# Performance work log

Hardware: AMD Instinct MI355X
Metric: run time of the kernel (lower is better)

The kernel has to match this reference:

```python
import jax, jax.numpy as jnp
import numpy as np

CUTOFF = 5.0
COULOMB_CONSTANT = 14.3996454784936  # eV * Angstrom / e^2
SQRT2 = 1.4142135623730951
N_NODES = 500000
N_EDGES = 16000000


def polynomial_cutoff(r, cutoff):
    ratio = r / cutoff
    f = 1.0 - 6.0 * ratio**5 + 15.0 * ratio**4 - 10.0 * ratio**3
    return jnp.where(r <= cutoff, f, 0.0)


def setup_inputs() -> dict:
    key = jax.random.key(0)
    k1, k2, k3, k4, k5 = jax.random.split(key, 5)
    charge = jax.random.normal(k1, (N_NODES,), dtype=jnp.float32)
    # sigma in (0.5, 1.5): positive Gaussian widths
    sigma = jax.random.uniform(k2, (N_NODES,), dtype=jnp.float32) + 0.5
    # bond_dist in (0.1, CUTOFF)
    bond_dist = jax.random.uniform(k3, (N_EDGES,), dtype=jnp.float32) * (CUTOFF - 0.1) + 0.1
    src = jax.random.randint(k4, (N_EDGES,), 0, N_NODES, dtype=jnp.int32)
    dst = jax.random.randint(k5, (N_EDGES,), 0, N_NODES, dtype=jnp.int32)
    return {"charge": charge, "sigma": sigma, "bond_dist": bond_dist, "src": src, "dst": dst}


def reference(charge, sigma, bond_dist, src, dst):
    # Edge-wise message: q_dst * erf(r / (sqrt2 * gamma)) * fcut(r) / r * K
    gamma = jnp.sqrt(sigma[src] ** 2 + sigma[dst] ** 2)  # [E]
    msg = (
        charge[dst]
        * jax.scipy.special.erf(bond_dist / (SQRT2 * gamma))
        * polynomial_cutoff(bond_dist, CUTOFF)
        / bond_dist
    ) * COULOMB_CONSTANT
    # Sum-aggregate messages at destination nodes (DGL fn.sum semantics)
    elec_pot = jax.ops.segment_sum(msg, dst, num_segments=charge.shape[0])
    return elec_pot
```

## Files before the change

### kernel.cpp

```cpp
#include <hip/hip_runtime.h>
#include <hip/hip_fp16.h>
#include <math.h>
#include <stdint.h>

#define CUTOFF_F     5.0f
#define INV_CUTOFF   0.2f
#define KCOUL        14.3996454784936f
#define INV_SQRT2    0.7071067811865475f

typedef int            vint4    __attribute__((ext_vector_type(4)));
typedef float          vfloat4  __attribute__((ext_vector_type(4)));
typedef uint32_t       vuint4   __attribute__((ext_vector_type(4)));
typedef unsigned short vushort8 __attribute__((ext_vector_type(8)));

#define WSHIFT        12
#define WINDOW        4096
#define NB            123
#define WGS_PER_B     8
#define NWG2          (NB * WGS_PER_B)
#define EPT           8
#define EPB           4096
#define OFFS_STRIDE   128
#define SPAN_MAX      512

__device__ __forceinline__ float erf_approx(float x) {
    const float a1 = 0.254829592f, a2 = -0.284496736f, a3 = 1.421413741f,
                a4 = -1.453152027f, a5 = 1.061405429f, p = 0.3275911f;
    float t = __builtin_amdgcn_rcpf(fmaf(p, x, 1.0f));
    float poly = t * fmaf(t, fmaf(t, fmaf(t, fmaf(t, a5, a4), a3), a2), a1);
    return 1.0f - poly * __expf(-x * x);
}

__device__ __forceinline__ float edge_val(float rr, float s2sum) {
    float inv_gamma = rsqrtf(s2sum);
    float x  = rr * INV_CUTOFF;
    float fc = fmaf(x * x * x, fmaf(x, fmaf(-6.0f, x, 15.0f), -10.0f), 1.0f);
    fc = (rr <= CUTOFF_F) ? fc : 0.0f;
    return erf_approx(rr * INV_SQRT2 * inv_gamma) * fc * KCOUL
         * __builtin_amdgcn_rcpf(rr);
}

__global__ __launch_bounds__(256, 6) void p1_bin(
    const float* __restrict__ bond,
    const int*   __restrict__ src,
    const int*   __restrict__ dst,
    unsigned short* __restrict__ offs,
    uint32_t*       __restrict__ sl_out,
    unsigned short* __restrict__ r_out,
    int n_edges)
{
    __shared__ uint32_t hist[NB];
    __shared__ uint32_t scan_s[NB + 1];
    __shared__ alignas(16) uint32_t       buf_sl[EPB];
    __shared__ alignas(16) unsigned short buf_r[EPB];

    const int tid = threadIdx.x;
    const int e0  = blockIdx.x * EPB;

    if (tid < NB) hist[tid] = 0;
    __syncthreads();

    int   dA[EPT], sA[EPT], dB[EPT], sB[EPT];
    float rA[EPT], rB[EPT];
    const bool full = (e0 + EPB <= n_edges);
    if (full) {
        const vint4*   dp = (const vint4*)(dst + e0) + tid;
        const vint4*   sp = (const vint4*)(src + e0) + tid;
        const vfloat4* rp = (const vfloat4*)(bond + e0) + tid;
        vint4 d0 = __builtin_nontemporal_load(dp);
        vint4 d1 = __builtin_nontemporal_load(dp + 256);
        vint4 s0 = __builtin_nontemporal_load(sp);
        vint4 s1 = __builtin_nontemporal_load(sp + 256);
        vfloat4 r0 = __builtin_nontemporal_load(rp);
        vfloat4 r1 = __builtin_nontemporal_load(rp + 256);
        vint4 d2 = __builtin_nontemporal_load(dp + 512);
        vint4 d3 = __builtin_nontemporal_load(dp + 768);
        vint4 s2 = __builtin_nontemporal_load(sp + 512);
        vint4 s3 = __builtin_nontemporal_load(sp + 768);
        vfloat4 r2 = __builtin_nontemporal_load(rp + 512);
        vfloat4 r3 = __builtin_nontemporal_load(rp + 768);
        dA[0]=d0.x; dA[1]=d0.y; dA[2]=d0.z; dA[3]=d0.w;
        dA[4]=d1.x; dA[5]=d1.y; dA[6]=d1.z; dA[7]=d1.w;
        sA[0]=s0.x; sA[1]=s0.y; sA[2]=s0.z; sA[3]=s0.w;
        sA[4]=s1.x; sA[5]=s1.y; sA[6]=s1.z; sA[7]=s1.w;
        rA[0]=r0.x; rA[1]=r0.y; rA[2]=r0.z; rA[3]=r0.w;
        rA[4]=r1.x; rA[5]=r1.y; rA[6]=r1.z; rA[7]=r1.w;
        dB[0]=d2.x; dB[1]=d2.y; dB[2]=d2.z; dB[3]=d2.w;
        dB[4]=d3.x; dB[5]=d3.y; dB[6]=d3.z; dB[7]=d3.w;
        sB[0]=s2.x; sB[1]=s2.y; sB[2]=s2.z; sB[3]=s2.w;
        sB[4]=s3.x; sB[5]=s3.y; sB[6]=s3.z; sB[7]=s3.w;
        rB[0]=r2.x; rB[1]=r2.y; rB[2]=r2.z; rB[3]=r2.w;
        rB[4]=r3.x; rB[5]=r3.y; rB[6]=r3.z; rB[7]=r3.w;
    } else {
        #pragma unroll
        for (int j = 0; j < EPT; ++j) {
            int eA = e0 + (j >> 2) * 1024 + tid * 4 + (j & 3);
            int eB = eA + 2048;
            if (eA < n_edges) { dA[j] = dst[eA]; sA[j] = src[eA]; rA[j] = bond[eA]; }
            else dA[j] = -1;
            if (eB < n_edges) { dB[j] = dst[eB]; sB[j] = src[eB]; rB[j] = bond[eB]; }
            else dB[j] = -1;
        }
    }

    uint32_t slA[EPT], brA[EPT], slB[EPT], brB[EPT];
    unsigned short hrA[EPT], hrB[EPT];
    #pragma unroll
    for (int j = 0; j < EPT; ++j) {
        if (dA[j] >= 0) {
            unsigned b = (unsigned)dA[j] >> WSHIFT;
            uint32_t r = atomicAdd(&hist[b], 1u);
            brA[j] = (b << 16) | r;
            slA[j] = ((uint32_t)sA[j] << WSHIFT) | ((unsigned)dA[j] & (WINDOW - 1));
            hrA[j] = __half_as_ushort(__float2half_rn(rA[j]));
        } else brA[j] = 0xFFFFFFFFu;
    }
    #pragma unroll
    for (int j = 0; j < EPT; ++j) {
        if (dB[j] >= 0) {
            unsigned b = (unsigned)dB[j] >> WSHIFT;
            uint32_t r = atomicAdd(&hist[b], 1u);
            brB[j] = (b << 16) | r;
            slB[j] = ((uint32_t)sB[j] << WSHIFT) | ((unsigned)dB[j] & (WINDOW - 1));
            hrB[j] = __half_as_ushort(__float2half_rn(rB[j]));
        } else brB[j] = 0xFFFFFFFFu;
    }
    __syncthreads();

    if (tid < 64) {
        int i0 = 2 * tid, i1 = 2 * tid + 1;
        uint32_t v0 = (i0 < NB) ? hist[i0] : 0u;
        uint32_t v1 = (i1 < NB) ? hist[i1] : 0u;
        uint32_t s  = v0 + v1;
        uint32_t inc = s;
        #pragma unroll
        for (int d = 1; d < 64; d <<= 1) {
            uint32_t up = __shfl_up(inc, d, 64);
            if (tid >= d) inc += up;
        }
        uint32_t excl = inc - s;
        if (i0 < NB) scan_s[i0] = excl;
        if (i1 < NB) scan_s[i1] = excl + v0;
        if (tid == 63) scan_s[NB] = inc;
    }
    __syncthreads();

    #pragma unroll
    for (int j = 0; j < EPT; ++j)
        if (brA[j] != 0xFFFFFFFFu) {
            uint32_t p = scan_s[brA[j] >> 16] + (brA[j] & 0xFFFFu);
            buf_sl[p] = slA[j]; buf_r[p] = hrA[j];
        }
    #pragma unroll
    for (int j = 0; j < EPT; ++j)
        if (brB[j] != 0xFFFFFFFFu) {
            uint32_t p = scan_s[brB[j] >> 16] + (brB[j] & 0xFFFFu);
            buf_sl[p] = slB[j]; buf_r[p] = hrB[j];
        }
    __syncthreads();

    if (tid <= NB)
        offs[(size_t)blockIdx.x * OFFS_STRIDE + tid] = (unsigned short)scan_s[tid];

    {
        const vuint4* bs = (const vuint4*)buf_sl;
        vuint4* os = (vuint4*)(sl_out + (size_t)blockIdx.x * EPB);
        #pragma unroll
        for (int i = 0; i < EPB / 4 / 256; ++i)
            __builtin_nontemporal_store(bs[tid + i * 256], os + tid + i * 256);
        const vushort8* br = (const vushort8*)buf_r;
        vushort8* orr = (vushort8*)(r_out + (size_t)blockIdx.x * EPB);
        #pragma unroll
        for (int i = 0; i < EPB / 8 / 256; ++i)
            __builtin_nontemporal_store(br[tid + i * 256], orr + tid + i * 256);
    }
}

__global__ __launch_bounds__(256) void p2_acc(
    const uint32_t*       __restrict__ sl_in,
    const unsigned short* __restrict__ r_in,
    const unsigned short* __restrict__ offs,
    const float*          __restrict__ sigma,
    float*                __restrict__ partials,
    int n_nodes, int nblk)
{
    __shared__ float acc[WINDOW];
    __shared__ float sig[WINDOW];
    __shared__ unsigned short offLo[SPAN_MAX];
    __shared__ unsigned short offHi[SPAN_MAX];

    const int g = blockIdx.x;
    const int b = g / WGS_PER_B;
    const int w = g % WGS_PER_B;

    vfloat4* accv = (vfloat4*)acc;
    for (int i = threadIdx.x; i < WINDOW / 4; i += 256)
        accv[i] = (vfloat4){0.f, 0.f, 0.f, 0.f};

    const int nbase  = b << WSHIFT;
    const int nvalid = (n_nodes - nbase < WINDOW) ? (n_nodes - nbase) : WINDOW;
    if (nvalid == WINDOW) {
        vfloat4* sv = (vfloat4*)sig;
        const vfloat4* gp = (const vfloat4*)(sigma + nbase);
        for (int i = threadIdx.x; i < WINDOW / 4; i += 256) sv[i] = gp[i];
    } else {
        for (int i = threadIdx.x; i < WINDOW; i += 256)
            sig[i] = (i < nvalid) ? sigma[nbase + i] : 0.f;
    }

    const int span = (nblk + WGS_PER_B - 1) / WGS_PER_B;
    const int blk0 = w * span;
    int blkN = nblk - blk0;
    if (blkN > span) blkN = span;
    if (blkN < 0) blkN = 0;
    for (int i = threadIdx.x; i < blkN; i += 256) {
        size_t o = (size_t)(blk0 + i) * OFFS_STRIDE + b;
        offLo[i] = offs[o];
        offHi[i] = offs[o + 1];
    }
    __syncthreads();

    const int wave = threadIdx.x >> 6, lane = threadIdx.x & 63;
    for (int i = wave; i < blkN; i += 4) {
        uint32_t lo  = offLo[i];
        uint32_t len = (uint32_t)offHi[i] - lo;
        const uint32_t*       slb = sl_in + (size_t)(blk0 + i) * EPB + lo;
        const unsigned short* rb  = r_in  + (size_t)(blk0 + i) * EPB + lo;
        for (uint32_t k = lane; k < len; k += 64) {
            uint32_t sl = slb[k];
            float rr = __half2float(__ushort_as_half(rb[k]));
            float ss = sigma[sl >> WSHIFT];
            float sd = sig[sl & (WINDOW - 1)];
            float v  = edge_val(rr, fmaf(ss, ss, sd * sd));
            atomicAdd(&acc[sl & (WINDOW - 1)], v);
        }
    }
    __syncthreads();

    vfloat4* outp = (vfloat4*)(partials + (size_t)g * WINDOW);
    for (int i = threadIdx.x; i < WINDOW / 4; i += 256)
        __builtin_nontemporal_store(accv[i], outp + i);
}

__global__ __launch_bounds__(256) void p3_reduce(
    const float* __restrict__ partials,
    const float* __restrict__ charge,
    float*       __restrict__ out, int n_nodes)
{
    int n = blockIdx.x * 256 + threadIdx.x;
    if (n >= n_nodes) return;
    unsigned b     = (unsigned)n >> WSHIFT;
    unsigned local = (unsigned)n & (WINDOW - 1);
    const float* p = partials + ((size_t)b * WGS_PER_B) * WINDOW + local;
    float sum = 0.0f;
    #pragma unroll
    for (int w = 0; w < WGS_PER_B; ++w)
        sum += __builtin_nontemporal_load(p + (size_t)w * WINDOW);
    out[n] = charge[n] * sum;
}

__global__ __launch_bounds__(256) void edge_msg_atomic(
    const float* __restrict__ charge, const float* __restrict__ sigma,
    const float* __restrict__ bond, const int* __restrict__ src,
    const int* __restrict__ dst, float* __restrict__ out, int n_edges)
{
    int i = blockIdx.x * blockDim.x + threadIdx.x;
    if (i < n_edges) {
        float ss = sigma[src[i]], sd = sigma[dst[i]];
        float msg = charge[dst[i]] * edge_val(bond[i], fmaf(ss, ss, sd * sd));
        atomicAdd(&out[dst[i]], msg);
    }
}

extern "C" void kernel_launch(void* const* d_in, const int* in_sizes, int n_in,
                              void* d_out, int out_size, void* d_ws, size_t ws_size,
                              hipStream_t stream) {
    const float* charge = (const float*)d_in[0];
    const float* sigma  = (const float*)d_in[1];
    const float* bond   = (const float*)d_in[2];
    const int*   src    = (const int*)d_in[3];
    const int*   dst    = (const int*)d_in[4];
    float* out = (float*)d_out;

    int n_nodes = in_sizes[0];
    int n_edges = in_sizes[2];

    int nblk = (n_edges + EPB - 1) / EPB;
    int span = (nblk + WGS_PER_B - 1) / WGS_PER_B;

    size_t offs_b = (size_t)nblk * OFFS_STRIDE * sizeof(unsigned short);
    size_t sl_b   = (size_t)nblk * EPB * sizeof(uint32_t);
    size_t r_b    = (size_t)nblk * EPB * sizeof(unsigned short);
    size_t part_b = (size_t)NWG2 * WINDOW * sizeof(float);
    size_t need   = offs_b + sl_b + r_b + part_b;

    if (n_nodes <= NB * WINDOW && need <= ws_size && span <= SPAN_MAX) {
        unsigned short* offs = (unsigned short*)d_ws;
        uint32_t*       slp  = (uint32_t*)((char*)d_ws + offs_b);
        unsigned short* rp   = (unsigned short*)((char*)d_ws + offs_b + sl_b);
        float* partial = (float*)((char*)d_ws + offs_b + sl_b + r_b);

        p1_bin<<<nblk, 256, 0, stream>>>(bond, src, dst, offs, slp, rp, n_edges);
        p2_acc<<<NWG2, 256, 0, stream>>>(slp, rp, offs, sigma, partial,
                                         n_nodes, nblk);
        int blocks3 = (n_nodes + 255) / 256;
        p3_reduce<<<blocks3, 256, 0, stream>>>(partial, charge, out, n_nodes);
    } else {
        (void)hipMemsetAsync(out, 0, (size_t)n_nodes * sizeof(float), stream);
        int blocks = (n_edges + 255) / 256;
        edge_msg_atomic<<<blocks, 256, 0, stream>>>(charge, sigma, bond, src, dst,
                                                    out, n_edges);
    }
}
```

Measured before the change: 346.6 us.

## Flatten p2 edge loop via prefix-sum and binary search, double workgroups per bucket

The per-wave loop over source blocks with short, uneven segments is replaced by a flat loop over all edges of the workgroup's span. Each thread finds its source block by binary search over a prefix sum of segment lengths, which should fix lane underuse on short segments. Workgroups per bucket go from 8 to 16, sigma is read from global memory instead of being staged in LDS, and launch bounds now ask for 8 blocks per CU to raise occupancy. The costs are more partials for p3 to reduce, an 8-step binary search per edge, and uncached global sigma gathers.

```diff
diff --git a/kernel.cpp b/kernel.cpp
--- a/kernel.cpp
+++ b/kernel.cpp
@@ -16,12 +16,12 @@
 #define WSHIFT        12
 #define WINDOW        4096
 #define NB            123
-#define WGS_PER_B     8
+#define WGS_PER_B     16
 #define NWG2          (NB * WGS_PER_B)
 #define EPT           8
 #define EPB           4096
 #define OFFS_STRIDE   128
-#define SPAN_MAX      512
+#define SPAN_MAX      256
 
 __device__ __forceinline__ float erf_approx(float x) {
     const float a1 = 0.254829592f, a2 = -0.284496736f, a3 = 1.421413741f,
@@ -176,7 +176,7 @@
     }
 }
 
-__global__ __launch_bounds__(256) void p2_acc(
+__global__ __launch_bounds__(256, 8) void p2_acc(
     const uint32_t*       __restrict__ sl_in,
     const unsigned short* __restrict__ r_in,
     const unsigned short* __restrict__ offs,
@@ -185,28 +185,17 @@
     int n_nodes, int nblk)
 {
     __shared__ float acc[WINDOW];
-    __shared__ float sig[WINDOW];
-    __shared__ unsigned short offLo[SPAN_MAX];
-    __shared__ unsigned short offHi[SPAN_MAX];
+    __shared__ unsigned short offLo_s[SPAN_MAX];
+    __shared__ uint32_t pref[SPAN_MAX + 1];
 
     const int g = blockIdx.x;
     const int b = g / WGS_PER_B;
     const int w = g % WGS_PER_B;
+    const int nbase = b << WSHIFT;
 
     vfloat4* accv = (vfloat4*)acc;
     for (int i = threadIdx.x; i < WINDOW / 4; i += 256)
         accv[i] = (vfloat4){0.f, 0.f, 0.f, 0.f};
-
-    const int nbase  = b << WSHIFT;
-    const int nvalid = (n_nodes - nbase < WINDOW) ? (n_nodes - nbase) : WINDOW;
-    if (nvalid == WINDOW) {
-        vfloat4* sv = (vfloat4*)sig;
-        const vfloat4* gp = (const vfloat4*)(sigma + nbase);
-        for (int i = threadIdx.x; i < WINDOW / 4; i += 256) sv[i] = gp[i];
-    } else {
-        for (int i = threadIdx.x; i < WINDOW; i += 256)
-            sig[i] = (i < nvalid) ? sigma[nbase + i] : 0.f;
-    }
 
     const int span = (nblk + WGS_PER_B - 1) / WGS_PER_B;
     const int blk0 = w * span;
@@ -215,25 +204,49 @@
     if (blkN < 0) blkN = 0;
     for (int i = threadIdx.x; i < blkN; i += 256) {
         size_t o = (size_t)(blk0 + i) * OFFS_STRIDE + b;
-        offLo[i] = offs[o];
-        offHi[i] = offs[o + 1];
-    }
-    __syncthreads();
-
-    const int wave = threadIdx.x >> 6, lane = threadIdx.x & 63;
-    for (int i = wave; i < blkN; i += 4) {
-        uint32_t lo  = offLo[i];
-        uint32_t len = (uint32_t)offHi[i] - lo;
-        const uint32_t*       slb = sl_in + (size_t)(blk0 + i) * EPB + lo;
-        const unsigned short* rb  = r_in  + (size_t)(blk0 + i) * EPB + lo;
-        for (uint32_t k = lane; k < len; k += 64) {
-            uint32_t sl = slb[k];
-            float rr = __half2float(__ushort_as_half(rb[k]));
-            float ss = sigma[sl >> WSHIFT];
-            float sd = sig[sl & (WINDOW - 1)];
-            float v  = edge_val(rr, fmaf(ss, ss, sd * sd));
-            atomicAdd(&acc[sl & (WINDOW - 1)], v);
-        }
+        unsigned lo = offs[o], hi = offs[o + 1];
+        offLo_s[i] = (unsigned short)lo;
+        pref[i] = hi - lo;
+    }
+    __syncthreads();
+
+    if (threadIdx.x < 64) {
+        uint32_t carry = 0;
+        for (int c = 0; c < blkN; c += 64) {
+            int i = c + threadIdx.x;
+            uint32_t v = (i < blkN) ? pref[i] : 0u;
+            uint32_t inc = v;
+            #pragma unroll
+            for (int d = 1; d < 64; d <<= 1) {
+                uint32_t up = __shfl_up(inc, d, 64);
+                if ((int)threadIdx.x >= d) inc += up;
+            }
+            if (i < blkN) pref[i] = carry + inc - v;
+            carry += __shfl(inc, 63, 64);
+        }
+        if (threadIdx.x == 0) pref[blkN] = carry;
+    }
+    __syncthreads();
+
+    const uint32_t total = pref[blkN];
+
+    for (uint32_t idx = threadIdx.x; idx < total; idx += 256) {
+        int lo = 0, hi = blkN;
+        #pragma unroll
+        for (int s = 0; s < 8; ++s) {
+            int mid = (lo + hi) >> 1;
+            bool c = (pref[mid] <= idx);
+            lo = c ? mid : lo;
+            hi = c ? hi : mid;
+        }
+        uint32_t k = idx - pref[lo];
+        size_t addr = (size_t)(blk0 + lo) * EPB + offLo_s[lo] + k;
+        uint32_t sl = sl_in[addr];
+        float rr = __half2float(__ushort_as_half(r_in[addr]));
+        float ss = sigma[sl >> WSHIFT];
+        float sd = sigma[nbase + (sl & (WINDOW - 1))];
+        float v  = edge_val(rr, fmaf(ss, ss, sd * sd));
+        atomicAdd(&acc[sl & (WINDOW - 1)], v);
     }
     __syncthreads();
 
```

New measurement: 378.4 us. 9.2% more time.
